# Kernel tuning notes

Measured on AMD Instinct MI355X. Metric: run time of the kernel, lower is better.

Reference implementation:

```python
import jax, jax.numpy as jnp
import numpy as np

B, S1, S2, D1, D2 = 4, 2048, 2048, 512, 512
H, DK, DV = 8, 64, 64


def setup_inputs() -> dict:
    key = jax.random.key(0)
    ks = jax.random.split(key, 8)
    x1 = jax.random.normal(ks[0], (B, S1, D1), dtype=jnp.float32)
    x2 = jax.random.normal(ks[1], (B, S2, D2), dtype=jnp.float32)
    x3 = jax.random.normal(ks[2], (B, S2, D2), dtype=jnp.float32)
    s = 0.02
    Wq = jax.random.normal(ks[3], (D1, H * DK), dtype=jnp.float32) * s
    Wk = jax.random.normal(ks[4], (D2, H * DK), dtype=jnp.float32) * s
    Wv = jax.random.normal(ks[5], (D2, H * DV), dtype=jnp.float32) * s
    Wo = jax.random.normal(ks[6], (H * DV, D1), dtype=jnp.float32) * s
    bo = jnp.zeros((D1,), dtype=jnp.float32)
    return {"x1": x1, "x2": x2, "x3": x3, "Wq": Wq, "Wk": Wk, "Wv": Wv, "Wo": Wo, "bo": bo}


def reference(x1, x2, x3, Wq, Wk, Wv, Wo, bo):
    b, s1, _ = x1.shape
    # project to per-head q, k, v: [B, H, S, Dh]
    q = (x1 @ Wq).reshape(b, s1, H, DK).transpose(0, 2, 1, 3)
    k = (x2 @ Wk).reshape(b, x2.shape[1], H, DK).transpose(0, 2, 1, 3)
    v = (x3 @ Wv).reshape(b, x3.shape[1], H, DV).transpose(0, 2, 1, 3)
    scores = jnp.einsum('bhqd,bhkd->bhqk', q, k) / jnp.sqrt(jnp.float32(DK))
    attn = jax.nn.softmax(scores, axis=-1)
    out = jnp.einsum('bhqk,bhkd->bhqd', attn, v)  # [B, H, S1, DV]
    out = out.transpose(0, 2, 1, 3).reshape(b, s1, H * DV)
    return out @ Wo + bo
```

## Files before the change

### kernel.cpp

```cpp
#include <hip/hip_runtime.h>

typedef __attribute__((ext_vector_type(4))) float f32x4;
typedef __attribute__((ext_vector_type(8))) __bf16 bf16x8;
typedef __attribute__((ext_vector_type(4))) __bf16 bf16x4;

#define DEVINL __device__ __forceinline__

DEVINL void gld16(const void* g, void* l) {
  __builtin_amdgcn_global_load_lds((__attribute__((address_space(1))) void*)(void*)g,
                                   (__attribute__((address_space(3))) void*)l, 16, 0, 0);
}


__global__ __launch_bounds__(256) void cvt_x(const float* x1, const float* x2, const float* x3,
                                             __bf16* o0, __bf16* o1, __bf16* o2) {
  const int z = blockIdx.y;
  const float* s = z == 0 ? x1 : z == 1 ? x2 : x3;
  __bf16* d = z == 0 ? o0 : z == 1 ? o1 : o2;
  size_t i = (size_t)blockIdx.x * 256 + threadIdx.x;
  f32x4 v = ((const f32x4*)s)[i];
  bf16x4 o;
#pragma unroll
  for (int j = 0; j < 4; ++j) o[j] = (__bf16)v[j];
  ((bf16x4*)d)[i] = o;
}

__global__ __launch_bounds__(256) void cvt_w(const float* Wq, const float* Wk, const float* Wv,
                                             const float* Wo, __bf16* WT) {
  __shared__ float t[64][65];
  const int z = blockIdx.z;
  const float* W = z == 0 ? Wq : z == 1 ? Wk : z == 2 ? Wv : Wo;
  __bf16* D = WT + (size_t)z * 512 * 512;
  const int r0 = blockIdx.x * 64, c0 = blockIdx.y * 64;
  const int tx = threadIdx.x & 63, ty = threadIdx.x >> 6;
#pragma unroll
  for (int j = 0; j < 16; ++j)
    t[ty + j * 4][tx] = W[(size_t)(r0 + ty + j * 4) * 512 + c0 + tx];
  __syncthreads();
#pragma unroll
  for (int j = 0; j < 16; ++j)
    D[(size_t)(c0 + ty + j * 4) * 512 + r0 + tx] = (__bf16)t[tx][ty + j * 4];
}


DEVINL void gemm_tile(const __bf16* A, const __bf16* Bt, int m0, int n0,
                      __bf16* As, __bf16* Bs, f32x4 acc[4][4]) {
  const int tid = threadIdx.x, lane = tid & 63, w = tid >> 6;
  const int qd = lane >> 4, r = lane & 15;
  const int wm = w & 1, wn = w >> 1;
  const char* ap[4];
  const char* bp[4];
#pragma unroll
  for (int j = 0; j < 4; ++j) {
    int c = (w * 4 + j) * 64 + lane;
    int row = c >> 3, cs = c & 7;
    int gc = cs ^ (row & 7);
    ap[j] = (const char*)A + (size_t)(m0 + row) * 1024 + gc * 16;
    bp[j] = (const char*)Bt + (size_t)(n0 + row) * 1024 + gc * 16;
  }
  int offA[4][2], offB[4][2];
#pragma unroll
  for (int t = 0; t < 4; ++t)
#pragma unroll
    for (int ks = 0; ks < 2; ++ks) {
      int m = wm * 64 + t * 16 + r;
      offA[t][ks] = m * 128 + (((ks * 4 + qd) ^ (m & 7)) * 16);
      int n = wn * 64 + t * 16 + r;
      offB[t][ks] = n * 128 + (((ks * 4 + qd) ^ (n & 7)) * 16);
    }
  char* AsC = (char*)As;
  char* BsC = (char*)Bs;
  for (int kt = 0; kt < 8; ++kt) {
    __syncthreads();
#pragma unroll
    for (int j = 0; j < 4; ++j) {
      gld16(ap[j] + kt * 128, AsC + (w * 4 + j) * 1024);
      gld16(bp[j] + kt * 128, BsC + (w * 4 + j) * 1024);
    }
    __syncthreads();
#pragma unroll
    for (int ks = 0; ks < 2; ++ks) {
      bf16x8 a[4], b[4];
#pragma unroll
      for (int t = 0; t < 4; ++t) {
        a[t] = *(const bf16x8*)(AsC + offA[t][ks]);
        b[t] = *(const bf16x8*)(BsC + offB[t][ks]);
      }
#pragma unroll
      for (int i = 0; i < 4; ++i)
#pragma unroll
        for (int j2 = 0; j2 < 4; ++j2)
          acc[i][j2] = __builtin_amdgcn_mfma_f32_16x16x32_bf16(a[i], b[j2], acc[i][j2], 0, 0, 0);
    }
  }
}

__global__ __launch_bounds__(256, 2) void gemm_proj(const __bf16* x1b, const __bf16* x2b,
                                                    const __bf16* x3b, const __bf16* WT,
                                                    __bf16* Qo, __bf16* Ko, __bf16* Vto) {
  __shared__ __align__(16) char smem[34816];
  __bf16* As = (__bf16*)smem;
  __bf16* Bs = (__bf16*)(smem + 16384);
  const int z = blockIdx.z;
  const __bf16* A = z == 0 ? x1b : z == 1 ? x2b : x3b;
  const __bf16* Bt = WT + (size_t)z * 512 * 512;
  const int l = blockIdx.x;
  const int sidx = l >> 3;
  const int m0 = ((l & 7) * 8 + (sidx >> 2)) * 128;
  const int n0 = (sidx & 3) * 128;
  f32x4 acc[4][4] = {};
  gemm_tile(A, Bt, m0, n0, As, Bs, acc);
  const int tid = threadIdx.x, lane = tid & 63, w = tid >> 6;
  const int qd = lane >> 4, r = lane & 15, wm = w & 1, wn = w >> 1;
  const int b = m0 >> 11, sbase = m0 & 2047;
  if (z == 2) {
    __syncthreads();
    char* T = smem;
#pragma unroll
    for (int mt = 0; mt < 4; ++mt)
#pragma unroll
      for (int nt = 0; nt < 4; ++nt) {
        int dv = wn * 64 + nt * 16 + r;
        int sl = wm * 64 + mt * 16 + qd * 4;
        bf16x4 p4;
#pragma unroll
        for (int g = 0; g < 4; ++g) p4[g] = (__bf16)acc[mt][nt][g];
        *(bf16x4*)(T + (size_t)dv * 272 + sl * 2) = p4;
      }
    __syncthreads();
#pragma unroll
    for (int p2 = 0; p2 < 2; ++p2) {
      int dvrow = p2 * 64 + (tid >> 2);
      int col = n0 + dvrow, h = col >> 6, d = col & 63;
      __bf16* dst = Vto + ((size_t)(b * 8 + h) * 64 + d) * 2048 + sbase + (tid & 3) * 8;
#pragma unroll
      for (int j = 0; j < 4; ++j) {
        bf16x8 vv = *(const bf16x8*)(T + (size_t)dvrow * 272 + (tid & 3) * 16 + j * 64);
        *(bf16x8*)(dst + j * 32) = vv;
      }
    }
  } else {
    const float qscale = 0.18033688f;
#pragma unroll
    for (int mt = 0; mt < 4; ++mt) {
#pragma unroll
      for (int nt = 0; nt < 4; ++nt) {
        f32x4 v = acc[mt][nt];
        if (z == 0) {
#pragma unroll
          for (int g = 0; g < 4; ++g) v[g] *= qscale;
        }
        int col = n0 + wn * 64 + nt * 16 + r;
        int h = col >> 6, d = col & 63;
        int s = sbase + wm * 64 + mt * 16 + qd * 4;
        __bf16* O = (z == 0 ? Qo : Ko) + ((size_t)(b * 8 + h) * 2048 + s) * 64 + d;
#pragma unroll
        for (int g = 0; g < 4; ++g) O[(size_t)g * 64] = (__bf16)v[g];
      }
    }
  }
}

__global__ __launch_bounds__(256, 2) void gemm_out(const __bf16* Ob, const __bf16* WoT,
                                                   const float* bo, float* out) {
  __shared__ __align__(16) __bf16 As[64 * 64];
  __shared__ __align__(16) __bf16 Bs[128 * 64];
  const int tid = threadIdx.x, lane = tid & 63, w = tid >> 6;
  const int qd = lane >> 4, r = lane & 15, wm = w & 1, wn = w >> 1;
  const int id = blockIdx.x;
  const int rest = id >> 3;
  const int m0 = ((id & 7) * 16 + (rest & 15)) * 64;
  const int n0 = (rest >> 4) * 128;
  const char* ap[2];
  const char* bp[4];
#pragma unroll
  for (int j = 0; j < 2; ++j) {
    int c = (w * 2 + j) * 64 + lane;
    int row = c >> 3, gc = (c & 7) ^ (row & 7);
    ap[j] = (const char*)Ob + (size_t)(m0 + row) * 1024 + gc * 16;
  }
#pragma unroll
  for (int j = 0; j < 4; ++j) {
    int c = (w * 4 + j) * 64 + lane;
    int row = c >> 3, gc = (c & 7) ^ (row & 7);
    bp[j] = (const char*)WoT + (size_t)(n0 + row) * 1024 + gc * 16;
  }
  int offA[2][2], offB[4][2];
#pragma unroll
  for (int ks = 0; ks < 2; ++ks) {
#pragma unroll
    for (int t = 0; t < 2; ++t) {
      int m = wm * 32 + t * 16 + r;
      offA[t][ks] = m * 128 + (((ks * 4 + qd) ^ (m & 7)) * 16);
    }
#pragma unroll
    for (int t = 0; t < 4; ++t) {
      int n = wn * 64 + t * 16 + r;
      offB[t][ks] = n * 128 + (((ks * 4 + qd) ^ (n & 7)) * 16);
    }
  }
  char* AsC = (char*)As;
  char* BsC = (char*)Bs;
  f32x4 acc[2][4] = {};
  for (int kt = 0; kt < 8; ++kt) {
    __syncthreads();
#pragma unroll
    for (int j = 0; j < 2; ++j) gld16(ap[j] + kt * 128, AsC + (w * 2 + j) * 1024);
#pragma unroll
    for (int j = 0; j < 4; ++j) gld16(bp[j] + kt * 128, BsC + (w * 4 + j) * 1024);
    __syncthreads();
#pragma unroll
    for (int ks = 0; ks < 2; ++ks) {
      bf16x8 a[2], b[4];
#pragma unroll
      for (int t = 0; t < 2; ++t) a[t] = *(const bf16x8*)(AsC + offA[t][ks]);
#pragma unroll
      for (int t = 0; t < 4; ++t) b[t] = *(const bf16x8*)(BsC + offB[t][ks]);
#pragma unroll
      for (int i = 0; i < 2; ++i)
#pragma unroll
        for (int j2 = 0; j2 < 4; ++j2)
          acc[i][j2] = __builtin_amdgcn_mfma_f32_16x16x32_bf16(a[i], b[j2], acc[i][j2], 0, 0, 0);
    }
  }
#pragma unroll
  for (int nt = 0; nt < 4; ++nt) {
    int col = n0 + wn * 64 + nt * 16 + r;
    float bv = bo[col];
#pragma unroll
    for (int mt = 0; mt < 2; ++mt) {
      int mg = m0 + wm * 32 + mt * 16 + qd * 4;
#pragma unroll
      for (int g = 0; g < 4; ++g) out[(size_t)(mg + g) * 512 + col] = acc[mt][nt][g] + bv;
    }
  }
}

__global__ __launch_bounds__(256, 3) void attn(const __bf16* Q, const __bf16* K,
                                               const __bf16* Vt, __bf16* Opart, float* Lp) {
  __shared__ __align__(16) __bf16 Qs[128 * 64];
  __shared__ __align__(16) __bf16 Ks[64 * 64];
  __shared__ __align__(16) __bf16 Vs[64 * 64];
  __shared__ __align__(16) __bf16 Ps[128 * 72];
  const int tid = threadIdx.x, lane = tid & 63, w = tid >> 6;
  const int qd = lane >> 4, r = lane & 15;
  const int id = blockIdx.x;
  const int rest = id >> 3;
  const int bh = (id & 7) * 4 + (rest >> 5);
  const int kvh = (rest >> 4) & 1;
  const int q0 = (rest & 15) * 128;
  const __bf16* Qg = Q + ((size_t)bh * 2048 + q0) * 64;
  const __bf16* Kg = K + (size_t)bh * 2048 * 64;
  const __bf16* Vg = Vt + (size_t)bh * 64 * 2048;
  char* QsC = (char*)Qs;
  char* KsC = (char*)Ks;
  char* VsC = (char*)Vs;
  char* PsC = (char*)Ps;

#pragma unroll
  for (int j = 0; j < 4; ++j) {
    int c = (w * 4 + j) * 64 + lane;
    int m = c >> 3, gc = (c & 7) ^ (m & 7);
    gld16((const char*)Qg + m * 128 + gc * 16, QsC + (w * 4 + j) * 1024);
  }
  __syncthreads();

  bf16x8 qf[2][2];
#pragma unroll
  for (int mt = 0; mt < 2; ++mt)
#pragma unroll
    for (int ks = 0; ks < 2; ++ks) {
      int m = w * 32 + mt * 16 + r;
      qf[mt][ks] = *(const bf16x8*)(QsC + m * 128 + ((ks * 4 + qd) ^ (m & 7)) * 16);
    }

  int offKV[4][2];
#pragma unroll
  for (int t = 0; t < 4; ++t)
#pragma unroll
    for (int ks = 0; ks < 2; ++ks) {
      int n = t * 16 + r;
      offKV[t][ks] = n * 128 + ((ks * 4 + qd) ^ (n & 7)) * 16;
    }

  f32x4 oacc[2][4] = {};
  float lpart[2] = {0.f, 0.f};

  const int kt0 = kvh * 16;
  for (int kt = kt0; kt < kt0 + 16; ++kt) {
    __syncthreads();
#pragma unroll
    for (int j = 0; j < 2; ++j) {
      int c = (w * 2 + j) * 64 + lane;
      int m = c >> 3, gc = (c & 7) ^ (m & 7);
      gld16((const char*)Kg + (size_t)(kt * 64 + m) * 128 + gc * 16, KsC + (w * 2 + j) * 1024);
      gld16((const char*)Vg + (size_t)m * 4096 + kt * 128 + gc * 16, VsC + (w * 2 + j) * 1024);
    }
    __syncthreads();

    f32x4 sf[2][4] = {};
#pragma unroll
    for (int nt = 0; nt < 4; ++nt) {
      bf16x8 kf0 = *(const bf16x8*)(KsC + offKV[nt][0]);
      bf16x8 kf1 = *(const bf16x8*)(KsC + offKV[nt][1]);
#pragma unroll
      for (int mt = 0; mt < 2; ++mt) {
        sf[mt][nt] = __builtin_amdgcn_mfma_f32_16x16x32_bf16(kf0, qf[mt][0], sf[mt][nt], 0, 0, 0);
        sf[mt][nt] = __builtin_amdgcn_mfma_f32_16x16x32_bf16(kf1, qf[mt][1], sf[mt][nt], 0, 0, 0);
      }
    }
#pragma unroll
    for (int mt = 0; mt < 2; ++mt) {
      int q = w * 32 + mt * 16 + r;
#pragma unroll
      for (int nt = 0; nt < 4; ++nt) {
        bf16x4 p4;
#pragma unroll
        for (int g = 0; g < 4; ++g) {
          float p = __builtin_exp2f(sf[mt][nt][g]);
          lpart[mt] += p;
          p4[g] = (__bf16)p;
        }
        *(bf16x4*)(PsC + q * 144 + nt * 32 + qd * 8) = p4;
      }
    }
#pragma unroll
    for (int mt = 0; mt < 2; ++mt) {
      int prow = w * 32 + mt * 16 + r;
      bf16x8 pf0 = *(const bf16x8*)(PsC + prow * 144 + qd * 16);
      bf16x8 pf1 = *(const bf16x8*)(PsC + prow * 144 + 64 + qd * 16);
#pragma unroll
      for (int dvt = 0; dvt < 4; ++dvt) {
        bf16x8 vf0 = *(const bf16x8*)(VsC + offKV[dvt][0]);
        bf16x8 vf1 = *(const bf16x8*)(VsC + offKV[dvt][1]);
        oacc[mt][dvt] = __builtin_amdgcn_mfma_f32_16x16x32_bf16(pf0, vf0, oacc[mt][dvt], 0, 0, 0);
        oacc[mt][dvt] = __builtin_amdgcn_mfma_f32_16x16x32_bf16(pf1, vf1, oacc[mt][dvt], 0, 0, 0);
      }
    }
  }

  const size_t pbase = (size_t)(kvh * 32 + bh) * 2048;
#pragma unroll
  for (int mt = 0; mt < 2; ++mt) {
    float lsum = lpart[mt];
    lsum += __shfl_xor(lsum, 16, 64);
    lsum += __shfl_xor(lsum, 32, 64);
    if (lane < 16) Lp[pbase + q0 + w * 32 + mt * 16 + r] = lsum;
  }
  __bf16* Ob0 = Opart + pbase * 64;
#pragma unroll
  for (int mt = 0; mt < 2; ++mt) {
#pragma unroll
    for (int g = 0; g < 4; ++g) {
      int s = q0 + w * 32 + mt * 16 + qd * 4 + g;
#pragma unroll
      for (int dvt = 0; dvt < 4; ++dvt)
        Ob0[(size_t)s * 64 + dvt * 16 + r] = (__bf16)oacc[mt][dvt][g];
    }
  }
}

__global__ __launch_bounds__(256) void combine(const __bf16* Op, const float* Lp, __bf16* Ob) {
  int c = blockIdx.x * 256 + threadIdx.x;
  int bhs = c >> 3;
  int dv0 = (c & 7) * 8;
  size_t e = (size_t)bhs * 64 + dv0;
  bf16x8 a = *(const bf16x8*)(Op + e);
  bf16x8 b2 = *(const bf16x8*)(Op + ((size_t)32 * 2048 * 64) + e);
  float inv = 1.0f / (Lp[bhs] + Lp[bhs + 65536]);
  int bh = bhs >> 11, s = bhs & 2047, b = bh >> 3, h = bh & 7;
  bf16x8 o;
#pragma unroll
  for (int j = 0; j < 8; ++j) o[j] = (__bf16)(((float)a[j] + (float)b2[j]) * inv);
  *(bf16x8*)(Ob + ((size_t)(b * 2048 + s)) * 512 + h * 64 + dv0) = o;
}


extern "C" void kernel_launch(void* const* d_in, const int* in_sizes, int n_in,
                              void* d_out, int out_size, void* d_ws, size_t ws_size,
                              hipStream_t stream) {
  const float* x1 = (const float*)d_in[0];
  const float* x2 = (const float*)d_in[1];
  const float* x3 = (const float*)d_in[2];
  const float* Wq = (const float*)d_in[3];
  const float* Wk = (const float*)d_in[4];
  const float* Wv = (const float*)d_in[5];
  const float* Wo = (const float*)d_in[6];
  const float* bo = (const float*)d_in[7];
  float* out = (float*)d_out;
  char* ws = (char*)d_ws;
  const size_t MB = 1ull << 20;
  __bf16* x1b = (__bf16*)(ws);
  __bf16* x2b = (__bf16*)(ws + 8 * MB);
  __bf16* x3b = (__bf16*)(ws + 16 * MB);
  __bf16* WT = (__bf16*)(ws + 24 * MB);
  __bf16* Qb = (__bf16*)(ws + 26 * MB);
  __bf16* Kb = (__bf16*)(ws + 34 * MB);
  __bf16* Vtb = (__bf16*)(ws + 42 * MB);
  __bf16* Ob = (__bf16*)(ws + 50 * MB);
  __bf16* Opart = (__bf16*)(ws + 58 * MB);
  float* Lp = (float*)(ws + 74 * MB);

  cvt_x<<<dim3(4096, 3), 256, 0, stream>>>(x1, x2, x3, x1b, x2b, x3b);
  cvt_w<<<dim3(8, 8, 4), 256, 0, stream>>>(Wq, Wk, Wv, Wo, WT);
  gemm_proj<<<dim3(256, 1, 3), 256, 0, stream>>>(x1b, x2b, x3b, WT, Qb, Kb, Vtb);
  attn<<<dim3(1024), 256, 0, stream>>>(Qb, Kb, Vtb, Opart, Lp);
  combine<<<dim3(2048), 256, 0, stream>>>(Opart, Lp, Ob);
  gemm_out<<<dim3(512), 256, 0, stream>>>(Ob, WT + 3ull * 512 * 512, bo, out);
}
```

Baseline: 201.5 us.

## Merge conversion kernels, reuse Q smem for P, sum rows via MFMA, raise occupancy

Fuses the activation-cast and weight-transpose kernels into one launch, removing one kernel launch. In attention, P is written into the Q shared buffer with an XOR swizzle instead of a separate padded buffer, which cuts LDS use so the launch bound can go from 3 to 4 blocks. The row sums of P are now computed with an extra MFMA against a vector of ones instead of scalar adds and shuffles. gemm_proj's launch bound is also raised to 3, which may force register spills. Summing the bf16-rounded P values instead of fp32 values slightly changes the normalisation.

```diff
diff --git a/kernel.cpp b/kernel.cpp
--- a/kernel.cpp
+++ b/kernel.cpp
@@ -12,34 +12,37 @@
 }
 
 
-__global__ __launch_bounds__(256) void cvt_x(const float* x1, const float* x2, const float* x3,
-                                             __bf16* o0, __bf16* o1, __bf16* o2) {
-  const int z = blockIdx.y;
-  const float* s = z == 0 ? x1 : z == 1 ? x2 : x3;
-  __bf16* d = z == 0 ? o0 : z == 1 ? o1 : o2;
-  size_t i = (size_t)blockIdx.x * 256 + threadIdx.x;
-  f32x4 v = ((const f32x4*)s)[i];
-  bf16x4 o;
-#pragma unroll
-  for (int j = 0; j < 4; ++j) o[j] = (__bf16)v[j];
-  ((bf16x4*)d)[i] = o;
-}
-
-__global__ __launch_bounds__(256) void cvt_w(const float* Wq, const float* Wk, const float* Wv,
-                                             const float* Wo, __bf16* WT) {
+__global__ __launch_bounds__(256) void cvt_all(const float* x1, const float* x2, const float* x3,
+                                               const float* Wq, const float* Wk, const float* Wv,
+                                               const float* Wo, __bf16* o0, __bf16* o1, __bf16* o2,
+                                               __bf16* WT) {
   __shared__ float t[64][65];
-  const int z = blockIdx.z;
-  const float* W = z == 0 ? Wq : z == 1 ? Wk : z == 2 ? Wv : Wo;
-  __bf16* D = WT + (size_t)z * 512 * 512;
-  const int r0 = blockIdx.x * 64, c0 = blockIdx.y * 64;
-  const int tx = threadIdx.x & 63, ty = threadIdx.x >> 6;
-#pragma unroll
-  for (int j = 0; j < 16; ++j)
-    t[ty + j * 4][tx] = W[(size_t)(r0 + ty + j * 4) * 512 + c0 + tx];
-  __syncthreads();
-#pragma unroll
-  for (int j = 0; j < 16; ++j)
-    D[(size_t)(c0 + ty + j * 4) * 512 + r0 + tx] = (__bf16)t[tx][ty + j * 4];
+  const int bx = blockIdx.x;
+  if (bx < 12288) {
+    const int z = bx >> 12;
+    const float* s = z == 0 ? x1 : z == 1 ? x2 : x3;
+    __bf16* d = z == 0 ? o0 : z == 1 ? o1 : o2;
+    size_t i = (size_t)(bx & 4095) * 256 + threadIdx.x;
+    f32x4 v = ((const f32x4*)s)[i];
+    bf16x4 o;
+#pragma unroll
+    for (int j = 0; j < 4; ++j) o[j] = (__bf16)v[j];
+    ((bf16x4*)d)[i] = o;
+  } else {
+    const int l = bx - 12288;
+    const int z = l >> 6;
+    const float* W = z == 0 ? Wq : z == 1 ? Wk : z == 2 ? Wv : Wo;
+    __bf16* D = WT + (size_t)z * 512 * 512;
+    const int r0 = ((l >> 3) & 7) * 64, c0 = (l & 7) * 64;
+    const int tx = threadIdx.x & 63, ty = threadIdx.x >> 6;
+#pragma unroll
+    for (int j = 0; j < 16; ++j)
+      t[ty + j * 4][tx] = W[(size_t)(r0 + ty + j * 4) * 512 + c0 + tx];
+    __syncthreads();
+#pragma unroll
+    for (int j = 0; j < 16; ++j)
+      D[(size_t)(c0 + ty + j * 4) * 512 + r0 + tx] = (__bf16)t[tx][ty + j * 4];
+  }
 }
 
 
@@ -95,7 +98,7 @@
   }
 }
 
-__global__ __launch_bounds__(256, 2) void gemm_proj(const __bf16* x1b, const __bf16* x2b,
+__global__ __launch_bounds__(256, 3) void gemm_proj(const __bf16* x1b, const __bf16* x2b,
                                                     const __bf16* x3b, const __bf16* WT,
                                                     __bf16* Qo, __bf16* Ko, __bf16* Vto) {
   __shared__ __align__(16) char smem[34816];
@@ -236,12 +239,11 @@
   }
 }
 
-__global__ __launch_bounds__(256, 3) void attn(const __bf16* Q, const __bf16* K,
+__global__ __launch_bounds__(256, 4) void attn(const __bf16* Q, const __bf16* K,
                                                const __bf16* Vt, __bf16* Opart, float* Lp) {
-  __shared__ __align__(16) __bf16 Qs[128 * 64];
+  __shared__ __align__(16) __bf16 QPs[128 * 64];
   __shared__ __align__(16) __bf16 Ks[64 * 64];
   __shared__ __align__(16) __bf16 Vs[64 * 64];
-  __shared__ __align__(16) __bf16 Ps[128 * 72];
   const int tid = threadIdx.x, lane = tid & 63, w = tid >> 6;
   const int qd = lane >> 4, r = lane & 15;
   const int id = blockIdx.x;
@@ -252,16 +254,15 @@
   const __bf16* Qg = Q + ((size_t)bh * 2048 + q0) * 64;
   const __bf16* Kg = K + (size_t)bh * 2048 * 64;
   const __bf16* Vg = Vt + (size_t)bh * 64 * 2048;
-  char* QsC = (char*)Qs;
+  char* PsC = (char*)QPs;
   char* KsC = (char*)Ks;
   char* VsC = (char*)Vs;
-  char* PsC = (char*)Ps;
 
 #pragma unroll
   for (int j = 0; j < 4; ++j) {
     int c = (w * 4 + j) * 64 + lane;
     int m = c >> 3, gc = (c & 7) ^ (m & 7);
-    gld16((const char*)Qg + m * 128 + gc * 16, QsC + (w * 4 + j) * 1024);
+    gld16((const char*)Qg + m * 128 + gc * 16, PsC + (w * 4 + j) * 1024);
   }
   __syncthreads();
 
@@ -271,7 +272,7 @@
 #pragma unroll
     for (int ks = 0; ks < 2; ++ks) {
       int m = w * 32 + mt * 16 + r;
-      qf[mt][ks] = *(const bf16x8*)(QsC + m * 128 + ((ks * 4 + qd) ^ (m & 7)) * 16);
+      qf[mt][ks] = *(const bf16x8*)(PsC + m * 128 + ((ks * 4 + qd) ^ (m & 7)) * 16);
     }
 
   int offKV[4][2];
@@ -283,8 +284,12 @@
       offKV[t][ks] = n * 128 + ((ks * 4 + qd) ^ (n & 7)) * 16;
     }
 
+  bf16x8 ones;
+#pragma unroll
+  for (int j = 0; j < 8; ++j) ones[j] = (__bf16)1.0f;
+
   f32x4 oacc[2][4] = {};
-  float lpart[2] = {0.f, 0.f};
+  f32x4 lacc[2] = {};
 
   const int kt0 = kvh * 16;
   for (int kt = kt0; kt < kt0 + 16; ++kt) {
@@ -316,19 +321,17 @@
       for (int nt = 0; nt < 4; ++nt) {
         bf16x4 p4;
 #pragma unroll
-        for (int g = 0; g < 4; ++g) {
-          float p = __builtin_exp2f(sf[mt][nt][g]);
-          lpart[mt] += p;
-          p4[g] = (__bf16)p;
-        }
-        *(bf16x4*)(PsC + q * 144 + nt * 32 + qd * 8) = p4;
+        for (int g = 0; g < 4; ++g) p4[g] = (__bf16)__builtin_exp2f(sf[mt][nt][g]);
+        *(bf16x4*)(PsC + q * 128 + (((2 * nt + (qd >> 1)) ^ (q & 7)) * 16) + (qd & 1) * 8) = p4;
       }
     }
 #pragma unroll
     for (int mt = 0; mt < 2; ++mt) {
-      int prow = w * 32 + mt * 16 + r;
-      bf16x8 pf0 = *(const bf16x8*)(PsC + prow * 144 + qd * 16);
-      bf16x8 pf1 = *(const bf16x8*)(PsC + prow * 144 + 64 + qd * 16);
+      int q = w * 32 + mt * 16 + r;
+      bf16x8 pf0 = *(const bf16x8*)(PsC + q * 128 + ((qd ^ (q & 7)) * 16));
+      bf16x8 pf1 = *(const bf16x8*)(PsC + q * 128 + (((4 + qd) ^ (q & 7)) * 16));
+      lacc[mt] = __builtin_amdgcn_mfma_f32_16x16x32_bf16(pf0, ones, lacc[mt], 0, 0, 0);
+      lacc[mt] = __builtin_amdgcn_mfma_f32_16x16x32_bf16(pf1, ones, lacc[mt], 0, 0, 0);
 #pragma unroll
       for (int dvt = 0; dvt < 4; ++dvt) {
         bf16x8 vf0 = *(const bf16x8*)(VsC + offKV[dvt][0]);
@@ -342,10 +345,11 @@
   const size_t pbase = (size_t)(kvh * 32 + bh) * 2048;
 #pragma unroll
   for (int mt = 0; mt < 2; ++mt) {
-    float lsum = lpart[mt];
-    lsum += __shfl_xor(lsum, 16, 64);
-    lsum += __shfl_xor(lsum, 32, 64);
-    if (lane < 16) Lp[pbase + q0 + w * 32 + mt * 16 + r] = lsum;
+    if (r == 0) {
+#pragma unroll
+      for (int g = 0; g < 4; ++g)
+        Lp[pbase + q0 + w * 32 + mt * 16 + qd * 4 + g] = lacc[mt][g];
+    }
   }
   __bf16* Ob0 = Opart + pbase * 64;
 #pragma unroll
@@ -401,8 +405,7 @@
   __bf16* Opart = (__bf16*)(ws + 58 * MB);
   float* Lp = (float*)(ws + 74 * MB);
 
-  cvt_x<<<dim3(4096, 3), 256, 0, stream>>>(x1, x2, x3, x1b, x2b, x3b);
-  cvt_w<<<dim3(8, 8, 4), 256, 0, stream>>>(Wq, Wk, Wv, Wo, WT);
+  cvt_all<<<dim3(12544), 256, 0, stream>>>(x1, x2, x3, Wq, Wk, Wv, Wo, x1b, x2b, x3b, WT);
   gemm_proj<<<dim3(256, 1, 3), 256, 0, stream>>>(x1b, x2b, x3b, WT, Qb, Kb, Vtb);
   attn<<<dim3(1024), 256, 0, stream>>>(Qb, Kb, Vtb, Opart, Lp);
   combine<<<dim3(2048), 256, 0, stream>>>(Opart, Lp, Ob);
```

Result: faster. 183.2 us (-9.1%).
